# Performance work log

Measured on AMD Instinct MI355X. Metric: run time of the kernel, lower is better.

## Reference

```python
import jax, jax.numpy as jnp
import numpy as np

N_NODES = 100000


def gcn_conv(x, edge_index, W, b):
    """PyG GCNConv: h = x @ W; out = D^-1/2 (A+I) D^-1/2 h + b."""
    n = x.shape[0]
    src, dst = edge_index[0], edge_index[1]
    loop = jnp.arange(n)
    src = jnp.concatenate([src, loop])  # add self-loops
    dst = jnp.concatenate([dst, loop])
    # degree at target nodes (unit edge weights)
    deg = jax.ops.segment_sum(jnp.ones(dst.shape[0], dtype=x.dtype), dst, num_segments=n)
    dinv = jnp.where(deg > 0, jax.lax.rsqrt(deg), 0.0)
    norm = dinv[src] * dinv[dst]  # [E+n]
    h = x @ W  # [n, out]
    msg = h[src] * norm[:, None]  # gather + scale
    out = jax.ops.segment_sum(msg, dst, num_segments=n)  # scatter-add
    return out + b


def setup_inputs() -> dict:
    key = jax.random.key(0)
    k1, k2, k3, k4, k5, k6 = jax.random.split(key, 6)
    E = 3200000
    x = jax.random.normal(k1, (N_NODES, 2), dtype=jnp.float32)
    edge_index = jax.random.randint(k2, (2, E), 0, N_NODES, dtype=jnp.int64)
    W1 = jax.random.normal(k3, (2, 16), dtype=jnp.float32) * 0.5
    b1 = jax.random.normal(k4, (16,), dtype=jnp.float32) * 0.1
    W2 = jax.random.normal(k5, (16, 2), dtype=jnp.float32) * 0.25
    b2 = jax.random.normal(k6, (2,), dtype=jnp.float32) * 0.1
    return {"x": x, "edge_index": edge_index, "W1": W1, "b1": b1, "W2": W2, "b2": b2}


def reference(x, edge_index, W1, b1, W2, b2):
    h = jax.nn.relu(gcn_conv(x, edge_index, W1, b1))
    # dropout is identity at inference
    out = gcn_conv(h, edge_index, W2, b2)
    return jax.nn.log_softmax(out, axis=1)
```

## Files before the change

### kernel.cpp

```cpp
#include <hip/hip_runtime.h>
#include <math.h>


constexpr int N = 100000;
constexpr int NC = 49;
constexpr int CB = 2048;
constexpr int CAP1 = 68608;
constexpr int BSP = 512;
constexpr int ECHUNK = 8192;
constexpr int EPT = ECHUNK / BSP;
constexpr int MAXCH = 9;

__global__ __launch_bounds__(BSP) void k_pass1(const int* __restrict__ src,
                                               const int* __restrict__ dst, int E,
                                               int* __restrict__ gfill1,
                                               int* __restrict__ slotsC) {
    __shared__ int hist[NC];
    __shared__ int base[NC];
    int t = threadIdx.x;
    if (t < NC) hist[t] = 0;
    __syncthreads();
    int s[EPT], d[EPT];
    int ebase = blockIdx.x * ECHUNK + t * EPT;
#pragma unroll
    for (int k = 0; k < EPT / 4; k++) {
        int idx = ebase + 4 * k;
        if (idx + 3 < E) {
            *(int4*)(s + 4 * k) = *(const int4*)(src + idx);
            *(int4*)(d + 4 * k) = *(const int4*)(dst + idx);
        } else {
            for (int j = 0; j < 4; j++) {
                s[4 * k + j] = (idx + j < E) ? src[idx + j] : -1;
                d[4 * k + j] = (idx + j < E) ? dst[idx + j] : -1;
            }
        }
    }
#pragma unroll
    for (int k = 0; k < EPT; k++)
        if (d[k] >= 0) atomicAdd(&hist[d[k] >> 11], 1);
    __syncthreads();
    if (t < NC) {
        int c = hist[t];
        base[t] = c ? atomicAdd(&gfill1[t], c) : 0;
        hist[t] = 0;
    }
    __syncthreads();
#pragma unroll
    for (int k = 0; k < EPT; k++) {
        if (d[k] >= 0) {
            int bin = d[k] >> 11;
            int r = atomicAdd(&hist[bin], 1);
            int pos = base[bin] + r;
            if (pos < CAP1) slotsC[bin * CAP1 + pos] = (s[k] << 11) | (d[k] & 2047);
        }
    }
}

__global__ __launch_bounds__(BSP) void k_deg(const int* __restrict__ gfill1,
                                             const int* __restrict__ slotsC,
                                             int* __restrict__ degPart) {
    __shared__ int dh[CB];
    int c = blockIdx.x / MAXCH, j = blockIdx.x % MAXCH;
    int fill = min(gfill1[c], CAP1);
    int e0 = j * ECHUNK;
    if (e0 >= fill) return;
    int e1 = min(fill, e0 + ECHUNK);
    int t = threadIdx.x;
    for (int i = t; i < CB; i += BSP) dh[i] = 0;
    __syncthreads();
    const int* row = slotsC + c * CAP1;
    int v[EPT];
    int ebase = e0 + t * EPT;
#pragma unroll
    for (int k = 0; k < EPT / 4; k++) {
        int idx = ebase + 4 * k;
        if (idx + 3 < e1) {
            *(int4*)(v + 4 * k) = *(const int4*)(row + idx);
        } else {
            for (int jj = 0; jj < 4; jj++) v[4 * k + jj] = (idx + jj < e1) ? row[idx + jj] : -1;
        }
    }
#pragma unroll
    for (int k = 0; k < EPT; k++)
        if (v[k] >= 0) atomicAdd(&dh[v[k] & (CB - 1)], 1);
    __syncthreads();
    int* dp = degPart + blockIdx.x * CB;
    for (int i = t; i < CB; i += BSP) dp[i] = dh[i];
}

__global__ __launch_bounds__(256) void k_dinv(const int* __restrict__ gfill1,
                                              const int* __restrict__ degPart,
                                              const float* __restrict__ x,
                                              float* __restrict__ dinv,
                                              float2* __restrict__ sx) {
    int node = blockIdx.x * 256 + threadIdx.x;
    if (node >= N) return;
    int c = node >> 11, i = node & (CB - 1);
    int nch = (min(gfill1[c], CAP1) + ECHUNK - 1) / ECHUNK;
    const int* p = degPart + c * MAXCH * CB + i;
    int deg = 0;
    for (int j = 0; j < nch; j++) deg += p[j * CB];
    float di = rsqrtf((float)(deg + 1));
    dinv[node] = di;
    float2 xv = ((const float2*)x)[node];
    sx[node] = make_float2(xv.x * di, xv.y * di);
}

__global__ __launch_bounds__(BSP) void k_aggc(const int* __restrict__ gfill1,
                                              const int* __restrict__ slotsC,
                                              const float2* __restrict__ vals,
                                              float* __restrict__ partX,
                                              float* __restrict__ partY) {
    __shared__ float aX[CB], aY[CB];
    int c = blockIdx.x / MAXCH, j = blockIdx.x % MAXCH;
    int fill = min(gfill1[c], CAP1);
    int e0 = j * ECHUNK;
    if (e0 >= fill) return;
    int e1 = min(fill, e0 + ECHUNK);
    int t = threadIdx.x;
    for (int i = t; i < CB; i += BSP) { aX[i] = 0.f; aY[i] = 0.f; }
    __syncthreads();
    const int* row = slotsC + c * CAP1;
    int v[EPT];
    int ebase = e0 + t * EPT;
#pragma unroll
    for (int k = 0; k < EPT / 4; k++) {
        int idx = ebase + 4 * k;
        if (idx + 3 < e1) {
            *(int4*)(v + 4 * k) = *(const int4*)(row + idx);
        } else {
            for (int jj = 0; jj < 4; jj++) v[4 * k + jj] = (idx + jj < e1) ? row[idx + jj] : -1;
        }
    }
    float2 g[EPT];
#pragma unroll
    for (int k = 0; k < EPT; k++) g[k] = (v[k] >= 0) ? vals[v[k] >> 11] : make_float2(0.f, 0.f);
#pragma unroll
    for (int k = 0; k < EPT; k++) {
        if (v[k] >= 0) {
            int d = v[k] & (CB - 1);
            atomicAdd(&aX[d], g[k].x);
            atomicAdd(&aY[d], g[k].y);
        }
    }
    __syncthreads();
    float* px = partX + blockIdx.x * CB;
    float* py = partY + blockIdx.x * CB;
    for (int i = t; i < CB; i += BSP) { px[i] = aX[i]; py[i] = aY[i]; }
}

__global__ __launch_bounds__(256) void k_comb1(const int* __restrict__ gfill1,
                                               const float* __restrict__ partX,
                                               const float* __restrict__ partY,
                                               const float* __restrict__ dinv,
                                               const float2* __restrict__ sx,
                                               const float* __restrict__ W1,
                                               const float* __restrict__ b1,
                                               const float* __restrict__ W2,
                                               float2* __restrict__ sz) {
    __shared__ float sW1[32], sb1[16], sW2[32];
    int t = threadIdx.x;
    if (t < 32) sW1[t] = W1[t];
    else if (t < 48) sb1[t - 32] = b1[t - 32];
    else if (t < 80) sW2[t - 48] = W2[t - 48];
    __syncthreads();
    int node = blockIdx.x * 256 + t;
    if (node >= N) return;
    int c = node >> 11, i = node & (CB - 1);
    int nch = (min(gfill1[c], CAP1) + ECHUNK - 1) / ECHUNK;
    const float* px = partX + c * MAXCH * CB + i;
    const float* py = partY + c * MAXCH * CB + i;
    float ax = 0.f, ay = 0.f;
    for (int j = 0; j < nch; j++) { ax += px[j * CB]; ay += py[j * CB]; }
    float di = dinv[node];
    float2 sv = sx[node];
    float a0 = (ax + sv.x) * di;
    float a1 = (ay + sv.y) * di;
    float z0 = 0.f, z1 = 0.f;
#pragma unroll
    for (int k = 0; k < 16; k++) {
        float h = fmaf(a0, sW1[k], fmaf(a1, sW1[16 + k], sb1[k]));
        h = fmaxf(h, 0.f);
        z0 = fmaf(h, sW2[2 * k + 0], z0);
        z1 = fmaf(h, sW2[2 * k + 1], z1);
    }
    sz[node] = make_float2(z0 * di, z1 * di);
}

__global__ __launch_bounds__(256) void k_comb2(const int* __restrict__ gfill1,
                                               const float* __restrict__ partX,
                                               const float* __restrict__ partY,
                                               const float* __restrict__ dinv,
                                               const float2* __restrict__ sz,
                                               const float* __restrict__ b2,
                                               float2* __restrict__ out) {
    int node = blockIdx.x * 256 + threadIdx.x;
    if (node >= N) return;
    int c = node >> 11, i = node & (CB - 1);
    int nch = (min(gfill1[c], CAP1) + ECHUNK - 1) / ECHUNK;
    const float* px = partX + c * MAXCH * CB + i;
    const float* py = partY + c * MAXCH * CB + i;
    float ax = 0.f, ay = 0.f;
    for (int j = 0; j < nch; j++) { ax += px[j * CB]; ay += py[j * CB]; }
    float di = dinv[node];
    float2 sv = sz[node];
    float v0 = fmaf(ax + sv.x, di, b2[0]);
    float v1 = fmaf(ay + sv.y, di, b2[1]);
    float m = fmaxf(v0, v1);
    float lse = m + logf(expf(v0 - m) + expf(v1 - m));
    out[node] = make_float2(v0 - lse, v1 - lse);
}

extern "C" void kernel_launch(void* const* d_in, const int* in_sizes, int n_in,
                              void* d_out, int out_size, void* d_ws, size_t ws_size,
                              hipStream_t stream) {
    const float* x  = (const float*)d_in[0];
    const int*   ei = (const int*)d_in[1];
    const float* W1 = (const float*)d_in[2];
    const float* b1 = (const float*)d_in[3];
    const float* W2 = (const float*)d_in[4];
    const float* b2 = (const float*)d_in[5];

    const int E = in_sizes[1] / 2;
    const int* src = ei;
    const int* dst = ei + E;
    const int GP = (E + ECHUNK - 1) / ECHUNK;
    const int GB = NC * MAXCH;
    const int GN = (N + 255) / 256;

    char* ws = (char*)d_ws;
    size_t off = 0;
    auto alloc = [&](size_t bytes) {
        char* p = ws + off;
        off += (bytes + 511) & ~size_t(511);
        return p;
    };
    int*    gfill1  = (int*)alloc(NC * sizeof(int));
    float*  dinv    = (float*)alloc(N * sizeof(float));
    float2* sx      = (float2*)alloc(N * sizeof(float2));
    float2* sz      = (float2*)alloc(N * sizeof(float2));
    int*    slotsC  = (int*)alloc((size_t)NC * CAP1 * sizeof(int));
    int*    degPart = (int*)alloc((size_t)GB * CB * sizeof(int));
    float*  partX   = (float*)alloc((size_t)GB * CB * sizeof(float));
    float*  partY   = (float*)alloc((size_t)GB * CB * sizeof(float));

    hipMemsetAsync(gfill1, 0, NC * sizeof(int), stream);

    k_pass1<<<GP, BSP, 0, stream>>>(src, dst, E, gfill1, slotsC);
    k_deg<<<GB, BSP, 0, stream>>>(gfill1, slotsC, degPart);
    k_dinv<<<GN, 256, 0, stream>>>(gfill1, degPart, x, dinv, sx);
    k_aggc<<<GB, BSP, 0, stream>>>(gfill1, slotsC, sx, partX, partY);
    k_comb1<<<GN, 256, 0, stream>>>(gfill1, partX, partY, dinv, sx, W1, b1, W2, sz);
    k_aggc<<<GB, BSP, 0, stream>>>(gfill1, slotsC, sz, partX, partY);
    k_comb2<<<GN, 256, 0, stream>>>(gfill1, partX, partY, dinv, sz, b2, (float2*)d_out);
}
```

Before: 221.3 us.

## Fuse degree counting into binning pass via global atomics; halve edge chunk sizes

Degree counting moves into the binning pass as global atomic increments on a per-node degree array. This removes the separate k_deg kernel and its partial-histogram reduction in k_dinv. Edge chunk sizes for the binning and aggregation kernels drop from 8192 to 4096, which doubles the block count and the number of partial rows that the combine kernels reduce. The cost is 3.2M scattered global atomics competing with the binning work, plus a larger memset.

```diff
diff --git a/kernel.cpp b/kernel.cpp
--- a/kernel.cpp
+++ b/kernel.cpp
@@ -6,24 +6,30 @@
 constexpr int NC = 49;
 constexpr int CB = 2048;
 constexpr int CAP1 = 68608;
-constexpr int BSP = 512;
-constexpr int ECHUNK = 8192;
-constexpr int EPT = ECHUNK / BSP;
-constexpr int MAXCH = 9;
-
-__global__ __launch_bounds__(BSP) void k_pass1(const int* __restrict__ src,
-                                               const int* __restrict__ dst, int E,
-                                               int* __restrict__ gfill1,
-                                               int* __restrict__ slotsC) {
+
+constexpr int B1 = 512;
+constexpr int EC1 = 4096;
+constexpr int EPT1 = EC1 / B1;
+
+constexpr int BA = 512;
+constexpr int ECA = 4096;
+constexpr int EPTA = ECA / BA;
+constexpr int MAXCHA = (CAP1 + ECA - 1) / ECA;
+
+__global__ __launch_bounds__(B1) void k_pass1(const int* __restrict__ src,
+                                              const int* __restrict__ dst, int E,
+                                              int* __restrict__ gfill1,
+                                              int* __restrict__ deg,
+                                              int* __restrict__ slotsC) {
     __shared__ int hist[NC];
     __shared__ int base[NC];
     int t = threadIdx.x;
     if (t < NC) hist[t] = 0;
     __syncthreads();
-    int s[EPT], d[EPT];
-    int ebase = blockIdx.x * ECHUNK + t * EPT;
-#pragma unroll
-    for (int k = 0; k < EPT / 4; k++) {
+    int s[EPT1], d[EPT1];
+    int ebase = blockIdx.x * EC1 + t * EPT1;
+#pragma unroll
+    for (int k = 0; k < EPT1 / 4; k++) {
         int idx = ebase + 4 * k;
         if (idx + 3 < E) {
             *(int4*)(s + 4 * k) = *(const int4*)(src + idx);
@@ -36,8 +42,11 @@
         }
     }
 #pragma unroll
-    for (int k = 0; k < EPT; k++)
-        if (d[k] >= 0) atomicAdd(&hist[d[k] >> 11], 1);
+    for (int k = 0; k < EPT1; k++)
+        if (d[k] >= 0) {
+            atomicAdd(&hist[d[k] >> 11], 1);
+            atomicAdd(&deg[d[k]], 1);
+        }
     __syncthreads();
     if (t < NC) {
         int c = hist[t];
@@ -46,7 +55,7 @@
     }
     __syncthreads();
 #pragma unroll
-    for (int k = 0; k < EPT; k++) {
+    for (int k = 0; k < EPT1; k++) {
         if (d[k] >= 0) {
             int bin = d[k] >> 11;
             int r = atomicAdd(&hist[bin], 1);
@@ -56,23 +65,37 @@
     }
 }
 
-__global__ __launch_bounds__(BSP) void k_deg(const int* __restrict__ gfill1,
+__global__ __launch_bounds__(256) void k_dinv(const int* __restrict__ deg,
+                                              const float* __restrict__ x,
+                                              float* __restrict__ dinv,
+                                              float2* __restrict__ sx) {
+    int node = blockIdx.x * 256 + threadIdx.x;
+    if (node >= N) return;
+    float di = rsqrtf((float)(deg[node] + 1));
+    dinv[node] = di;
+    float2 xv = ((const float2*)x)[node];
+    sx[node] = make_float2(xv.x * di, xv.y * di);
+}
+
+__global__ __launch_bounds__(BA) void k_aggc(const int* __restrict__ gfill1,
                                              const int* __restrict__ slotsC,
-                                             int* __restrict__ degPart) {
-    __shared__ int dh[CB];
-    int c = blockIdx.x / MAXCH, j = blockIdx.x % MAXCH;
+                                             const float2* __restrict__ vals,
+                                             float* __restrict__ partX,
+                                             float* __restrict__ partY) {
+    __shared__ float aX[CB], aY[CB];
+    int c = blockIdx.x / MAXCHA, j = blockIdx.x % MAXCHA;
     int fill = min(gfill1[c], CAP1);
-    int e0 = j * ECHUNK;
+    int e0 = j * ECA;
     if (e0 >= fill) return;
-    int e1 = min(fill, e0 + ECHUNK);
+    int e1 = min(fill, e0 + ECA);
     int t = threadIdx.x;
-    for (int i = t; i < CB; i += BSP) dh[i] = 0;
+    for (int i = t; i < CB; i += BA) { aX[i] = 0.f; aY[i] = 0.f; }
     __syncthreads();
     const int* row = slotsC + c * CAP1;
-    int v[EPT];
-    int ebase = e0 + t * EPT;
-#pragma unroll
-    for (int k = 0; k < EPT / 4; k++) {
+    int v[EPTA];
+    int ebase = e0 + t * EPTA;
+#pragma unroll
+    for (int k = 0; k < EPTA / 4; k++) {
         int idx = ebase + 4 * k;
         if (idx + 3 < e1) {
             *(int4*)(v + 4 * k) = *(const int4*)(row + idx);
@@ -80,63 +103,11 @@
             for (int jj = 0; jj < 4; jj++) v[4 * k + jj] = (idx + jj < e1) ? row[idx + jj] : -1;
         }
     }
-#pragma unroll
-    for (int k = 0; k < EPT; k++)
-        if (v[k] >= 0) atomicAdd(&dh[v[k] & (CB - 1)], 1);
-    __syncthreads();
-    int* dp = degPart + blockIdx.x * CB;
-    for (int i = t; i < CB; i += BSP) dp[i] = dh[i];
-}
-
-__global__ __launch_bounds__(256) void k_dinv(const int* __restrict__ gfill1,
-                                              const int* __restrict__ degPart,
-                                              const float* __restrict__ x,
-                                              float* __restrict__ dinv,
-                                              float2* __restrict__ sx) {
-    int node = blockIdx.x * 256 + threadIdx.x;
-    if (node >= N) return;
-    int c = node >> 11, i = node & (CB - 1);
-    int nch = (min(gfill1[c], CAP1) + ECHUNK - 1) / ECHUNK;
-    const int* p = degPart + c * MAXCH * CB + i;
-    int deg = 0;
-    for (int j = 0; j < nch; j++) deg += p[j * CB];
-    float di = rsqrtf((float)(deg + 1));
-    dinv[node] = di;
-    float2 xv = ((const float2*)x)[node];
-    sx[node] = make_float2(xv.x * di, xv.y * di);
-}
-
-__global__ __launch_bounds__(BSP) void k_aggc(const int* __restrict__ gfill1,
-                                              const int* __restrict__ slotsC,
-                                              const float2* __restrict__ vals,
-                                              float* __restrict__ partX,
-                                              float* __restrict__ partY) {
-    __shared__ float aX[CB], aY[CB];
-    int c = blockIdx.x / MAXCH, j = blockIdx.x % MAXCH;
-    int fill = min(gfill1[c], CAP1);
-    int e0 = j * ECHUNK;
-    if (e0 >= fill) return;
-    int e1 = min(fill, e0 + ECHUNK);
-    int t = threadIdx.x;
-    for (int i = t; i < CB; i += BSP) { aX[i] = 0.f; aY[i] = 0.f; }
-    __syncthreads();
-    const int* row = slotsC + c * CAP1;
-    int v[EPT];
-    int ebase = e0 + t * EPT;
-#pragma unroll
-    for (int k = 0; k < EPT / 4; k++) {
-        int idx = ebase + 4 * k;
-        if (idx + 3 < e1) {
-            *(int4*)(v + 4 * k) = *(const int4*)(row + idx);
-        } else {
-            for (int jj = 0; jj < 4; jj++) v[4 * k + jj] = (idx + jj < e1) ? row[idx + jj] : -1;
-        }
-    }
-    float2 g[EPT];
-#pragma unroll
-    for (int k = 0; k < EPT; k++) g[k] = (v[k] >= 0) ? vals[v[k] >> 11] : make_float2(0.f, 0.f);
-#pragma unroll
-    for (int k = 0; k < EPT; k++) {
+    float2 g[EPTA];
+#pragma unroll
+    for (int k = 0; k < EPTA; k++) g[k] = (v[k] >= 0) ? vals[v[k] >> 11] : make_float2(0.f, 0.f);
+#pragma unroll
+    for (int k = 0; k < EPTA; k++) {
         if (v[k] >= 0) {
             int d = v[k] & (CB - 1);
             atomicAdd(&aX[d], g[k].x);
@@ -146,7 +117,7 @@
     __syncthreads();
     float* px = partX + blockIdx.x * CB;
     float* py = partY + blockIdx.x * CB;
-    for (int i = t; i < CB; i += BSP) { px[i] = aX[i]; py[i] = aY[i]; }
+    for (int i = t; i < CB; i += BA) { px[i] = aX[i]; py[i] = aY[i]; }
 }
 
 __global__ __launch_bounds__(256) void k_comb1(const int* __restrict__ gfill1,
@@ -167,9 +138,9 @@
     int node = blockIdx.x * 256 + t;
     if (node >= N) return;
     int c = node >> 11, i = node & (CB - 1);
-    int nch = (min(gfill1[c], CAP1) + ECHUNK - 1) / ECHUNK;
-    const float* px = partX + c * MAXCH * CB + i;
-    const float* py = partY + c * MAXCH * CB + i;
+    int nch = (min(gfill1[c], CAP1) + ECA - 1) / ECA;
+    const float* px = partX + (size_t)c * MAXCHA * CB + i;
+    const float* py = partY + (size_t)c * MAXCHA * CB + i;
     float ax = 0.f, ay = 0.f;
     for (int j = 0; j < nch; j++) { ax += px[j * CB]; ay += py[j * CB]; }
     float di = dinv[node];
@@ -197,9 +168,9 @@
     int node = blockIdx.x * 256 + threadIdx.x;
     if (node >= N) return;
     int c = node >> 11, i = node & (CB - 1);
-    int nch = (min(gfill1[c], CAP1) + ECHUNK - 1) / ECHUNK;
-    const float* px = partX + c * MAXCH * CB + i;
-    const float* py = partY + c * MAXCH * CB + i;
+    int nch = (min(gfill1[c], CAP1) + ECA - 1) / ECA;
+    const float* px = partX + (size_t)c * MAXCHA * CB + i;
+    const float* py = partY + (size_t)c * MAXCHA * CB + i;
     float ax = 0.f, ay = 0.f;
     for (int j = 0; j < nch; j++) { ax += px[j * CB]; ay += py[j * CB]; }
     float di = dinv[node];
@@ -224,8 +195,8 @@
     const int E = in_sizes[1] / 2;
     const int* src = ei;
     const int* dst = ei + E;
-    const int GP = (E + ECHUNK - 1) / ECHUNK;
-    const int GB = NC * MAXCH;
+    const int GP = (E + EC1 - 1) / EC1;
+    const int GB = NC * MAXCHA;
     const int GN = (N + 255) / 256;
 
     char* ws = (char*)d_ws;
@@ -235,22 +206,21 @@
         off += (bytes + 511) & ~size_t(511);
         return p;
     };
-    int*    gfill1  = (int*)alloc(NC * sizeof(int));
-    float*  dinv    = (float*)alloc(N * sizeof(float));
-    float2* sx      = (float2*)alloc(N * sizeof(float2));
-    float2* sz      = (float2*)alloc(N * sizeof(float2));
-    int*    slotsC  = (int*)alloc((size_t)NC * CAP1 * sizeof(int));
-    int*    degPart = (int*)alloc((size_t)GB * CB * sizeof(int));
-    float*  partX   = (float*)alloc((size_t)GB * CB * sizeof(float));
-    float*  partY   = (float*)alloc((size_t)GB * CB * sizeof(float));
-
-    hipMemsetAsync(gfill1, 0, NC * sizeof(int), stream);
-
-    k_pass1<<<GP, BSP, 0, stream>>>(src, dst, E, gfill1, slotsC);
-    k_deg<<<GB, BSP, 0, stream>>>(gfill1, slotsC, degPart);
-    k_dinv<<<GN, 256, 0, stream>>>(gfill1, degPart, x, dinv, sx);
-    k_aggc<<<GB, BSP, 0, stream>>>(gfill1, slotsC, sx, partX, partY);
+    int*    gfill1 = (int*)alloc((64 + N) * sizeof(int));
+    int*    deg    = gfill1 + 64;
+    float*  dinv   = (float*)alloc(N * sizeof(float));
+    float2* sx     = (float2*)alloc(N * sizeof(float2));
+    float2* sz     = (float2*)alloc(N * sizeof(float2));
+    int*    slotsC = (int*)alloc((size_t)NC * CAP1 * sizeof(int));
+    float*  partX  = (float*)alloc((size_t)GB * CB * sizeof(float));
+    float*  partY  = (float*)alloc((size_t)GB * CB * sizeof(float));
+
+    hipMemsetAsync(gfill1, 0, (64 + N) * sizeof(int), stream);
+
+    k_pass1<<<GP, B1, 0, stream>>>(src, dst, E, gfill1, deg, slotsC);
+    k_dinv<<<GN, 256, 0, stream>>>(deg, x, dinv, sx);
+    k_aggc<<<GB, BA, 0, stream>>>(gfill1, slotsC, sx, partX, partY);
     k_comb1<<<GN, 256, 0, stream>>>(gfill1, partX, partY, dinv, sx, W1, b1, W2, sz);
-    k_aggc<<<GB, BSP, 0, stream>>>(gfill1, slotsC, sz, partX, partY);
+    k_aggc<<<GB, BA, 0, stream>>>(gfill1, slotsC, sz, partX, partY);
     k_comb2<<<GN, 256, 0, stream>>>(gfill1, partX, partY, dinv, sz, b2, (float2*)d_out);
 }
```

Measured after the change: 340.9 us. 1.54x slower.
